# Performance work log

Hardware: AMD Instinct MI355X
Metric: run time of the kernel (lower is better)

Reference implementation:

```python
import jax, jax.numpy as jnp
import numpy as np


def setup_inputs() -> dict:
    key = jax.random.key(0)
    ks = jax.random.split(key, 7)
    T, B, I, H = 512, 64, 256, 512
    s_ih = 1.0 / np.sqrt(H)
    return {
        "x": jax.random.normal(ks[0], (T, B, I), dtype=jnp.float32),
        "h0": jax.random.normal(ks[1], (B, H), dtype=jnp.float32),
        "c0": jax.random.normal(ks[2], (B, H), dtype=jnp.float32),
        "w_ih": jax.random.normal(ks[3], (4 * H, I), dtype=jnp.float32) * s_ih,
        "w_hh": jax.random.normal(ks[4], (4 * H, H), dtype=jnp.float32) * s_ih,
        "b_ih": jax.random.normal(ks[5], (4 * H,), dtype=jnp.float32) * s_ih,
        "b_hh": jax.random.normal(ks[6], (4 * H,), dtype=jnp.float32) * s_ih,
    }


def reference(x, h0, c0, w_ih, w_hh, b_ih, b_hh):
    # Precompute the input projection for all timesteps in one big GEMM:
    # [T,B,I] @ [I,4H] -> [T,B,4H]
    xg = jnp.einsum("tbi,gi->tbg", x, w_ih) + b_ih + b_hh

    H = h0.shape[-1]

    def step(carry, xg_t):
        h, c = carry
        gates = xg_t + h @ w_hh.T  # [B, 4H]
        i_g, f_g, g_g, o_g = jnp.split(gates, 4, axis=-1)
        i_g = jax.nn.sigmoid(i_g)
        f_g = jax.nn.sigmoid(f_g)
        g_g = jnp.tanh(g_g)
        o_g = jax.nn.sigmoid(o_g)
        c_new = f_g * c + i_g * g_g
        h_new = o_g * jnp.tanh(c_new)
        return (h_new, c_new), h_new

    (h_f, c_f), outputs = jax.lax.scan(step, (h0, c0), xg)
    return outputs, h_f, c_f
```

## Files before the change

### kernel.cpp

```cpp
#include <hip/hip_runtime.h>
#include <hip/hip_bf16.h>

typedef __attribute__((ext_vector_type(8))) _Float16 half8;
typedef __attribute__((ext_vector_type(4))) float floatx4;
typedef __attribute__((ext_vector_type(4))) unsigned uintx4;

#define NTS 512
#define NB  64
#define NI  256
#define NH  512
#define NWG 128
#define NTHR 256

#define LOSCALE 4096.0f
#define LOINV   (1.0f / 4096.0f)

static __device__ __forceinline__ void split8s(const float* p, half8& hi, half8& lo) {
  float4 a = *(const float4*)p;
  float4 b = *(const float4*)(p + 4);
  float v[8] = {a.x, a.y, a.z, a.w, b.x, b.y, b.z, b.w};
#pragma unroll
  for (int i = 0; i < 8; ++i) {
    _Float16 h = (_Float16)v[i];
    hi[i] = h;
    lo[i] = (_Float16)((v[i] - (float)h) * LOSCALE);
  }
}

static __device__ __forceinline__ unsigned pack_cell_e(float v, unsigned ep) {
  _Float16 h = (_Float16)v;
  _Float16 l = (_Float16)((v - (float)h) * LOSCALE);
  union { _Float16 f; unsigned short s; } uh, ul;
  uh.f = h; ul.f = l;
  unsigned lo = ((unsigned)ul.s & 0xFFFCu) | (ep & 3u);
  return (lo << 16) | (unsigned)uh.s;
}

static __device__ __forceinline__ uintx4 load_cx4(const unsigned* p) {
  uintx4 r;
  asm volatile("global_load_dwordx4 %0, %1, off sc0 sc1"
               : "=v"(r)
               : "v"((unsigned long long)p)
               : "memory");
  return r;
}

__global__ void __launch_bounds__(NTHR, 1) lstm_persist_v10(
    const float* __restrict__ x,
    const float* __restrict__ h0,
    const float* __restrict__ c0,
    const float* __restrict__ w_ih,
    const float* __restrict__ w_hh,
    const float* __restrict__ b_ih,
    const float* __restrict__ b_hh,
    float* __restrict__ out,
    unsigned* __restrict__ hbuf)
{
  const int wg   = blockIdx.x;
  const int mh   = wg >> 5;
  const int ng   = wg & 31;
  const int b0   = mh * 16;
  const int j0   = ng * 16;
  const int tid  = threadIdx.x;
  const int wv   = tid >> 6;
  const int lane = tid & 63;
  const int ln   = lane & 15;
  const int lq   = lane >> 4;
  const int gL   = ln >> 2;
  const int cL   = ln & 3;

  __shared__ uintx4    wlo[4][24][64];
  __shared__ unsigned  hstage[16][516];

  int row_l[4];
  {
    half8 ones, rowv;
#pragma unroll
    for (int i = 0; i < 8; ++i) { ones[i] = (_Float16)1.0f; rowv[i] = (_Float16)(float)ln; }
    floatx4 z = {0.f, 0.f, 0.f, 0.f};
    floatx4 p1 = __builtin_amdgcn_mfma_f32_16x16x32_f16(rowv, ones, z, 0, 0, 0);
#pragma unroll
    for (int r = 0; r < 4; ++r)
      row_l[r] = (int)(p1[r] * (1.0f / 32.0f) + 0.5f);
  }

  const int jg   = j0 + wv * 4 + cL;
  const int grow = gL * NH + jg;
  half8 whh_hi[16], wih_hi[8];
  {
#pragma unroll
    for (int s = 0; s < 16; ++s) {
      half8 lo;
      split8s(w_hh + (size_t)grow * NH + 32 * s + 8 * lq, whh_hi[s], lo);
      union { half8 h; uintx4 u; } cv; cv.h = lo;
      wlo[wv][s][lane] = cv.u;
    }
#pragma unroll
    for (int s = 0; s < 8; ++s) {
      half8 lo;
      split8s(w_ih + (size_t)grow * NI + 32 * s + 8 * lq, wih_hi[s], lo);
      union { half8 h; uintx4 u; } cv; cv.h = lo;
      wlo[wv][16 + s][lane] = cv.u;
    }
  }

  const float bias_i = b_ih[jg]          + b_hh[jg];
  const float bias_f = b_ih[NH + jg]     + b_hh[NH + jg];
  const float bias_g = b_ih[2 * NH + jg] + b_hh[2 * NH + jg];
  const float bias_o = b_ih[3 * NH + jg] + b_hh[3 * NH + jg];

  int   bg_r[4];
  float c_s[4];
#pragma unroll
  for (int r = 0; r < 4; ++r) {
    bg_r[r] = b0 + row_l[r];
    c_s[r]  = c0[bg_r[r] * NH + jg];
  }

  const int PAR = NB * NH;

  if (gL == 0) {
#pragma unroll
    for (int r = 0; r < 4; ++r)
      __hip_atomic_store(&hbuf[bg_r[r] * NH + jg], pack_cell_e(h0[bg_r[r] * NH + jg], 0u),
                         __ATOMIC_RELAXED, __HIP_MEMORY_SCOPE_AGENT);
  }

  const int arow = b0 + ln;
  const int srow = tid & 15;
  const int scb  = (tid >> 4) * 32;

  for (int t = 0; t < NTS; ++t) {
    floatx4 acc_x   = {0.f, 0.f, 0.f, 0.f};
    floatx4 accl_x1 = {0.f, 0.f, 0.f, 0.f};
    floatx4 accl_x2 = {0.f, 0.f, 0.f, 0.f};
#pragma unroll
    for (int s = 0; s < 8; ++s) {
      half8 xh, xl;
      split8s(x + ((size_t)t * NB + arow) * NI + 32 * s + 8 * lq, xh, xl);
      union { uintx4 u; half8 h; } wl; wl.u = wlo[wv][16 + s][lane];
      acc_x   = __builtin_amdgcn_mfma_f32_16x16x32_f16(xh, wih_hi[s], acc_x,   0, 0, 0);
      accl_x1 = __builtin_amdgcn_mfma_f32_16x16x32_f16(xl, wih_hi[s], accl_x1, 0, 0, 0);
      accl_x2 = __builtin_amdgcn_mfma_f32_16x16x32_f16(xh, wl.h,      accl_x2, 0, 0, 0);
    }

    {
      const unsigned* hb = hbuf + (t & 1) * PAR + (b0 + srow) * NH + scb;
      const unsigned em = (unsigned)((t >> 1) & 3) << 16;
      uintx4 hv[8];
#pragma unroll
      for (int q = 0; q < 8; ++q) hv[q] = load_cx4(hb + 4 * q);

      __syncthreads();

      unsigned pend = 0xFFu;
      for (;;) {
        asm volatile("s_waitcnt vmcnt(0)" ::: "memory");
#pragma unroll
        for (int q = 0; q < 8; ++q) {
          if (pend & (1u << q)) {
            uintx4 v = hv[q];
            unsigned bad = ((v[0] ^ em) | (v[1] ^ em) | (v[2] ^ em) | (v[3] ^ em))
                           & 0x00030000u;
            if (!bad) {
              *(uintx4*)&hstage[srow][scb + 4 * q] = v;
              pend &= ~(1u << q);
            }
          }
        }
        if (__ballot(pend != 0u) == 0ull) break;
#pragma unroll
        for (int q = 0; q < 8; ++q)
          if (pend & (1u << q)) hv[q] = load_cx4(hb + 4 * q);
      }
    }
    __syncthreads();

    floatx4 acc_h  = {0.f, 0.f, 0.f, 0.f}, acc_h2  = {0.f, 0.f, 0.f, 0.f};
    floatx4 accl_a = {0.f, 0.f, 0.f, 0.f}, accl_a2 = {0.f, 0.f, 0.f, 0.f};
    floatx4 accl_b = {0.f, 0.f, 0.f, 0.f}, accl_b2 = {0.f, 0.f, 0.f, 0.f};
#pragma unroll
    for (int s = 0; s < 16; ++s) {
      const uintx4* hp = (const uintx4*)&hstage[ln][32 * s + 8 * lq];
      uintx4 hA = hp[0], hB = hp[1];
      union { unsigned u[4]; half8 h; } Ah, Al;
      Ah.u[0] = __builtin_amdgcn_perm(hA[1], hA[0], 0x05040100u);
      Al.u[0] = __builtin_amdgcn_perm(hA[1], hA[0], 0x07060302u);
      Ah.u[1] = __builtin_amdgcn_perm(hA[3], hA[2], 0x05040100u);
      Al.u[1] = __builtin_amdgcn_perm(hA[3], hA[2], 0x07060302u);
      Ah.u[2] = __builtin_amdgcn_perm(hB[1], hB[0], 0x05040100u);
      Al.u[2] = __builtin_amdgcn_perm(hB[1], hB[0], 0x07060302u);
      Ah.u[3] = __builtin_amdgcn_perm(hB[3], hB[2], 0x05040100u);
      Al.u[3] = __builtin_amdgcn_perm(hB[3], hB[2], 0x07060302u);
      union { uintx4 u; half8 h; } wl; wl.u = wlo[wv][s][lane];
      if (s < 8) {
        acc_h  = __builtin_amdgcn_mfma_f32_16x16x32_f16(Ah.h, whh_hi[s], acc_h,  0, 0, 0);
        accl_a = __builtin_amdgcn_mfma_f32_16x16x32_f16(Al.h, whh_hi[s], accl_a, 0, 0, 0);
        accl_b = __builtin_amdgcn_mfma_f32_16x16x32_f16(Ah.h, wl.h,      accl_b, 0, 0, 0);
      } else {
        acc_h2  = __builtin_amdgcn_mfma_f32_16x16x32_f16(Ah.h, whh_hi[s], acc_h2,  0, 0, 0);
        accl_a2 = __builtin_amdgcn_mfma_f32_16x16x32_f16(Al.h, whh_hi[s], accl_a2, 0, 0, 0);
        accl_b2 = __builtin_amdgcn_mfma_f32_16x16x32_f16(Ah.h, wl.h,      accl_b2, 0, 0, 0);
      }
    }

    const int par1 = ((t + 1) & 1) * PAR;
    const unsigned ep1 = (unsigned)(((t + 1) >> 1) & 3);
    float hn[4];
#pragma unroll
    for (int r = 0; r < 4; ++r) {
      float hi_s = acc_x[r] + acc_h[r] + acc_h2[r];
      float lo_s = accl_x1[r] + accl_x2[r] + accl_a[r] + accl_a2[r]
                 + accl_b[r] + accl_b2[r];
      float pre = hi_s + lo_s * LOINV;
      float pb = __shfl_xor(pre, 4);
      float pc = __shfl_xor(pre, 8);
      float pd = __shfl_xor(pb, 8);
      const bool g1 = (gL & 1), g2 = (gL & 2) != 0;
      float xi = g2 ? (g1 ? pd : pc) : (g1 ? pb : pre);
      float xf = g2 ? (g1 ? pc : pd) : (g1 ? pre : pb);
      float xg = g2 ? (g1 ? pb : pre) : (g1 ? pd : pc);
      float xo = g2 ? (g1 ? pre : pb) : (g1 ? pc : pd);
      xi += bias_i; xf += bias_f; xg += bias_g; xo += bias_o;
      float ig = 1.f / (1.f + __expf(-xi));
      float fg = 1.f / (1.f + __expf(-xf));
      float gg = 2.f / (1.f + __expf(-2.f * xg)) - 1.f;
      float og = 1.f / (1.f + __expf(-xo));
      c_s[r] = fg * c_s[r] + ig * gg;
      float tc = 2.f / (1.f + __expf(-2.f * c_s[r])) - 1.f;
      hn[r] = og * tc;
    }

    if (gL == 0) {
#pragma unroll
      for (int r = 0; r < 4; ++r)
        __hip_atomic_store(&hbuf[par1 + bg_r[r] * NH + jg], pack_cell_e(hn[r], ep1),
                           __ATOMIC_RELAXED, __HIP_MEMORY_SCOPE_AGENT);
    }

    if (gL == 0) {
      if (t < NTS - 1) {
#pragma unroll
        for (int r = 0; r < 4; ++r)
          out[((size_t)t * NB + bg_r[r]) * NH + jg] = hn[r];
      } else {
        const size_t hf_off = (size_t)NTS * NB * NH;
#pragma unroll
        for (int r = 0; r < 4; ++r) {
          out[((size_t)t * NB + bg_r[r]) * NH + jg] = hn[r];
          out[hf_off + bg_r[r] * NH + jg] = hn[r];
          out[hf_off + (size_t)NB * NH + bg_r[r] * NH + jg] = c_s[r];
        }
      }
    }
  }
}

extern "C" void kernel_launch(void* const* d_in, const int* in_sizes, int n_in,
                              void* d_out, int out_size, void* d_ws, size_t ws_size,
                              hipStream_t stream) {
  const float* x    = (const float*)d_in[0];
  const float* h0   = (const float*)d_in[1];
  const float* c0   = (const float*)d_in[2];
  const float* w_ih = (const float*)d_in[3];
  const float* w_hh = (const float*)d_in[4];
  const float* b_ih = (const float*)d_in[5];
  const float* b_hh = (const float*)d_in[6];
  float* out = (float*)d_out;
  unsigned* hbuf = (unsigned*)d_ws;

  hipLaunchKernelGGL(lstm_persist_v10, dim3(NWG), dim3(NTHR), 0, stream,
                     x, h0, c0, w_ih, w_hh, b_ih, b_hh, out, hbuf);
}
```

Baseline: 3.036 ms.

## Halve workgroup count with 8-wave blocks, swizzled h staging, vectorized h stores

Reorganizes the persistent LSTM from 128 workgroups of 4 waves to 64 workgroups of 8 waves, each covering 32 hidden units. This halves the number of blocks that must poll the shared h buffer each step. The W_ih low half now lives in registers instead of LDS, and the h-buffer loads are issued before the x-projection so they overlap it. The LDS h staging uses an XOR swizzle to avoid bank conflicts, and the new h values are transposed with lane shuffles so each thread writes a 16-byte packed store to both hbuf and the output. The cost is higher register pressure, heavier per-block work, and a new way of mapping lanes to stored rows.

```diff
diff --git a/kernel.cpp b/kernel.cpp
--- a/kernel.cpp
+++ b/kernel.cpp
@@ -9,8 +9,8 @@
 #define NB  64
 #define NI  256
 #define NH  512
-#define NWG 128
-#define NTHR 256
+#define NWG 64
+#define NTHR 512
 
 #define LOSCALE 4096.0f
 #define LOINV   (1.0f / 4096.0f)
@@ -44,8 +44,13 @@
                : "memory");
   return r;
 }
-
-__global__ void __launch_bounds__(NTHR, 1) lstm_persist_v10(
+static __device__ __forceinline__ void store_cx4(unsigned* p, uintx4 v) {
+  asm volatile("global_store_dwordx4 %0, %1, off sc0 sc1"
+               :: "v"((unsigned long long)p), "v"(v)
+               : "memory");
+}
+
+__global__ void __launch_bounds__(NTHR, 2) lstm_persist_v11(
     const float* __restrict__ x,
     const float* __restrict__ h0,
     const float* __restrict__ c0,
@@ -57,10 +62,10 @@
     unsigned* __restrict__ hbuf)
 {
   const int wg   = blockIdx.x;
-  const int mh   = wg >> 5;
-  const int ng   = wg & 31;
+  const int mh   = wg >> 4;
+  const int ng   = wg & 15;
   const int b0   = mh * 16;
-  const int j0   = ng * 16;
+  const int j0   = ng * 32;
   const int tid  = threadIdx.x;
   const int wv   = tid >> 6;
   const int lane = tid & 63;
@@ -69,8 +74,8 @@
   const int gL   = ln >> 2;
   const int cL   = ln & 3;
 
-  __shared__ uintx4    wlo[4][24][64];
-  __shared__ unsigned  hstage[16][516];
+  __shared__ uintx4    wlo[8][15][64];
+  __shared__ unsigned  hstage[16][512];
 
   int row_l[4];
   {
@@ -85,23 +90,24 @@
   }
 
   const int jg   = j0 + wv * 4 + cL;
+  const int jb   = j0 + wv * 4;
   const int grow = gL * NH + jg;
-  half8 whh_hi[16], wih_hi[8];
+  half8 whh_hi[16], wih_hi[8], wih_lo[8], whh_lo15;
   {
 #pragma unroll
     for (int s = 0; s < 16; ++s) {
       half8 lo;
       split8s(w_hh + (size_t)grow * NH + 32 * s + 8 * lq, whh_hi[s], lo);
-      union { half8 h; uintx4 u; } cv; cv.h = lo;
-      wlo[wv][s][lane] = cv.u;
-    }
-#pragma unroll
-    for (int s = 0; s < 8; ++s) {
-      half8 lo;
-      split8s(w_ih + (size_t)grow * NI + 32 * s + 8 * lq, wih_hi[s], lo);
-      union { half8 h; uintx4 u; } cv; cv.h = lo;
-      wlo[wv][16 + s][lane] = cv.u;
-    }
+      if (s < 15) {
+        union { half8 h; uintx4 u; } cv; cv.h = lo;
+        wlo[wv][s][lane] = cv.u;
+      } else {
+        whh_lo15 = lo;
+      }
+    }
+#pragma unroll
+    for (int s = 0; s < 8; ++s)
+      split8s(w_ih + (size_t)grow * NI + 32 * s + 8 * lq, wih_hi[s], wih_lo[s]);
   }
 
   const float bias_i = b_ih[jg]          + b_hh[jg];
@@ -116,6 +122,8 @@
     bg_r[r] = b0 + row_l[r];
     c_s[r]  = c0[bg_r[r] * NH + jg];
   }
+  const int brow_st = b0 + ((cL == 0) ? row_l[0] : (cL == 1) ? row_l[1]
+                           : (cL == 2) ? row_l[2] : row_l[3]);
 
   const int PAR = NB * NH;
 
@@ -126,11 +134,16 @@
                          __ATOMIC_RELAXED, __HIP_MEMORY_SCOPE_AGENT);
   }
 
-  const int arow = b0 + ln;
-  const int srow = tid & 15;
-  const int scb  = (tid >> 4) * 32;
+  const int arow  = b0 + ln;
+  const int srow  = tid & 15;
+  const int qbase = (tid >> 4) * 4;
 
   for (int t = 0; t < NTS; ++t) {
+    const unsigned* hb = hbuf + (t & 1) * PAR + (b0 + srow) * NH + qbase * 4;
+    uintx4 hv[4];
+#pragma unroll
+    for (int q = 0; q < 4; ++q) hv[q] = load_cx4(hb + 4 * q);
+
     floatx4 acc_x   = {0.f, 0.f, 0.f, 0.f};
     floatx4 accl_x1 = {0.f, 0.f, 0.f, 0.f};
     floatx4 accl_x2 = {0.f, 0.f, 0.f, 0.f};
@@ -138,39 +151,34 @@
     for (int s = 0; s < 8; ++s) {
       half8 xh, xl;
       split8s(x + ((size_t)t * NB + arow) * NI + 32 * s + 8 * lq, xh, xl);
-      union { uintx4 u; half8 h; } wl; wl.u = wlo[wv][16 + s][lane];
       acc_x   = __builtin_amdgcn_mfma_f32_16x16x32_f16(xh, wih_hi[s], acc_x,   0, 0, 0);
       accl_x1 = __builtin_amdgcn_mfma_f32_16x16x32_f16(xl, wih_hi[s], accl_x1, 0, 0, 0);
-      accl_x2 = __builtin_amdgcn_mfma_f32_16x16x32_f16(xh, wl.h,      accl_x2, 0, 0, 0);
-    }
+      accl_x2 = __builtin_amdgcn_mfma_f32_16x16x32_f16(xh, wih_lo[s], accl_x2, 0, 0, 0);
+    }
+
+    __syncthreads();
 
     {
-      const unsigned* hb = hbuf + (t & 1) * PAR + (b0 + srow) * NH + scb;
       const unsigned em = (unsigned)((t >> 1) & 3) << 16;
-      uintx4 hv[8];
-#pragma unroll
-      for (int q = 0; q < 8; ++q) hv[q] = load_cx4(hb + 4 * q);
-
-      __syncthreads();
-
-      unsigned pend = 0xFFu;
+      unsigned pend = 0xFu;
       for (;;) {
         asm volatile("s_waitcnt vmcnt(0)" ::: "memory");
 #pragma unroll
-        for (int q = 0; q < 8; ++q) {
+        for (int q = 0; q < 4; ++q) {
           if (pend & (1u << q)) {
             uintx4 v = hv[q];
             unsigned bad = ((v[0] ^ em) | (v[1] ^ em) | (v[2] ^ em) | (v[3] ^ em))
                            & 0x00030000u;
             if (!bad) {
-              *(uintx4*)&hstage[srow][scb + 4 * q] = v;
+              const int slot = (qbase + q) ^ (srow & 7);
+              *(uintx4*)&hstage[srow][slot << 2] = v;
               pend &= ~(1u << q);
             }
           }
         }
         if (__ballot(pend != 0u) == 0ull) break;
 #pragma unroll
-        for (int q = 0; q < 8; ++q)
+        for (int q = 0; q < 4; ++q)
           if (pend & (1u << q)) hv[q] = load_cx4(hb + 4 * q);
       }
     }
@@ -181,8 +189,9 @@
     floatx4 accl_b = {0.f, 0.f, 0.f, 0.f}, accl_b2 = {0.f, 0.f, 0.f, 0.f};
 #pragma unroll
     for (int s = 0; s < 16; ++s) {
-      const uintx4* hp = (const uintx4*)&hstage[ln][32 * s + 8 * lq];
-      uintx4 hA = hp[0], hB = hp[1];
+      const int q0 = 8 * s + 2 * lq;
+      uintx4 hA = *(const uintx4*)&hstage[ln][(q0 ^ (ln & 7)) << 2];
+      uintx4 hB = *(const uintx4*)&hstage[ln][((q0 + 1) ^ (ln & 7)) << 2];
       union { unsigned u[4]; half8 h; } Ah, Al;
       Ah.u[0] = __builtin_amdgcn_perm(hA[1], hA[0], 0x05040100u);
       Al.u[0] = __builtin_amdgcn_perm(hA[1], hA[0], 0x07060302u);
@@ -192,15 +201,21 @@
       Al.u[2] = __builtin_amdgcn_perm(hB[1], hB[0], 0x07060302u);
       Ah.u[3] = __builtin_amdgcn_perm(hB[3], hB[2], 0x05040100u);
       Al.u[3] = __builtin_amdgcn_perm(hB[3], hB[2], 0x07060302u);
-      union { uintx4 u; half8 h; } wl; wl.u = wlo[wv][s][lane];
+      half8 wlh;
+      if (s < 15) {
+        union { uintx4 u; half8 h; } wl; wl.u = wlo[wv][s][lane];
+        wlh = wl.h;
+      } else {
+        wlh = whh_lo15;
+      }
       if (s < 8) {
         acc_h  = __builtin_amdgcn_mfma_f32_16x16x32_f16(Ah.h, whh_hi[s], acc_h,  0, 0, 0);
         accl_a = __builtin_amdgcn_mfma_f32_16x16x32_f16(Al.h, whh_hi[s], accl_a, 0, 0, 0);
-        accl_b = __builtin_amdgcn_mfma_f32_16x16x32_f16(Ah.h, wl.h,      accl_b, 0, 0, 0);
+        accl_b = __builtin_amdgcn_mfma_f32_16x16x32_f16(Ah.h, wlh,       accl_b, 0, 0, 0);
       } else {
         acc_h2  = __builtin_amdgcn_mfma_f32_16x16x32_f16(Ah.h, whh_hi[s], acc_h2,  0, 0, 0);
         accl_a2 = __builtin_amdgcn_mfma_f32_16x16x32_f16(Al.h, whh_hi[s], accl_a2, 0, 0, 0);
-        accl_b2 = __builtin_amdgcn_mfma_f32_16x16x32_f16(Ah.h, wl.h,      accl_b2, 0, 0, 0);
+        accl_b2 = __builtin_amdgcn_mfma_f32_16x16x32_f16(Ah.h, wlh,       accl_b2, 0, 0, 0);
       }
     }
 
@@ -231,19 +246,29 @@
       hn[r] = og * tc;
     }
 
-    if (gL == 0) {
-#pragma unroll
-      for (int r = 0; r < 4; ++r)
-        __hip_atomic_store(&hbuf[par1 + bg_r[r] * NH + jg], pack_cell_e(hn[r], ep1),
-                           __ATOMIC_RELAXED, __HIP_MEMORY_SCOPE_AGENT);
-    }
-
-    if (gL == 0) {
-      if (t < NTS - 1) {
-#pragma unroll
-        for (int r = 0; r < 4; ++r)
-          out[((size_t)t * NB + bg_r[r]) * NH + jg] = hn[r];
-      } else {
+    if (t < NTS - 1) {
+      const bool c0b = (lane & 1), c1b = (lane & 2) != 0;
+      float a0 = __shfl_xor(hn[1], 1), a1 = __shfl_xor(hn[0], 1);
+      float a2 = __shfl_xor(hn[3], 1), a3 = __shfl_xor(hn[2], 1);
+      float v10 = c0b ? a0 : hn[0], v11 = c0b ? hn[1] : a1;
+      float v12 = c0b ? a2 : hn[2], v13 = c0b ? hn[3] : a3;
+      float b0v = __shfl_xor(v12, 2), b1v = __shfl_xor(v13, 2);
+      float b2v = __shfl_xor(v10, 2), b3v = __shfl_xor(v11, 2);
+      float T0 = c1b ? b0v : v10, T1 = c1b ? b1v : v11;
+      float T2 = c1b ? v12 : b2v, T3 = c1b ? v13 : b3v;
+
+      if (gL == 0) {
+        uintx4 pk;
+        pk[0] = pack_cell_e(T0, ep1);
+        pk[1] = pack_cell_e(T1, ep1);
+        pk[2] = pack_cell_e(T2, ep1);
+        pk[3] = pack_cell_e(T3, ep1);
+        store_cx4(&hbuf[par1 + brow_st * NH + jb], pk);
+        floatx4 ov = {T0, T1, T2, T3};
+        *(floatx4*)&out[((size_t)t * NB + brow_st) * NH + jb] = ov;
+      }
+    } else {
+      if (gL == 0) {
         const size_t hf_off = (size_t)NTS * NB * NH;
 #pragma unroll
         for (int r = 0; r < 4; ++r) {
@@ -269,6 +294,6 @@
   float* out = (float*)d_out;
   unsigned* hbuf = (unsigned*)d_ws;
 
-  hipLaunchKernelGGL(lstm_persist_v10, dim3(NWG), dim3(NTHR), 0, stream,
+  hipLaunchKernelGGL(lstm_persist_v11, dim3(NWG), dim3(NTHR), 0, stream,
                      x, h0, c0, w_ih, w_hh, b_ih, b_hh, out, hbuf);
 }
```

After: 6.326 ms. 108% more time.

## Prefetch h before x-projection, double-buffer spin polls, vectorize h stores via shuffles

Applied to the files above, without the earlier changes.

The first poll of the previous-step hidden state is now issued before the input-projection MFMAs, so its latency overlaps that compute. The spin-wait alternates two in-flight batches of loads using vmcnt(8) instead of draining everything on each retry. Per-lane scalar atomic stores of h and out are replaced by a lane-shuffle transpose and one 16-byte store per lane with sc0 sc1 cache bits. This cuts cross-workgroup handoff latency and store count, at the cost of more outstanding loads, extra shuffles, and reliance on the packed epoch tags staying consistent within a dwordx4 store.

```diff
diff --git a/kernel.cpp b/kernel.cpp
--- a/kernel.cpp
+++ b/kernel.cpp
@@ -44,8 +44,13 @@
                : "memory");
   return r;
 }
-
-__global__ void __launch_bounds__(NTHR, 1) lstm_persist_v10(
+static __device__ __forceinline__ void store_cx4(unsigned* p, uintx4 v) {
+  asm volatile("global_store_dwordx4 %0, %1, off sc0 sc1"
+               :: "v"((unsigned long long)p), "v"(v)
+               : "memory");
+}
+
+__global__ void __launch_bounds__(NTHR, 1) lstm_persist_v16(
     const float* __restrict__ x,
     const float* __restrict__ h0,
     const float* __restrict__ c0,
@@ -85,6 +90,7 @@
   }
 
   const int jg   = j0 + wv * 4 + cL;
+  const int jb   = j0 + wv * 4;
   const int grow = gL * NH + jg;
   half8 whh_hi[16], wih_hi[8];
   {
@@ -116,6 +122,8 @@
     bg_r[r] = b0 + row_l[r];
     c_s[r]  = c0[bg_r[r] * NH + jg];
   }
+  const int brow_st = b0 + ((cL == 0) ? row_l[0] : (cL == 1) ? row_l[1]
+                           : (cL == 2) ? row_l[2] : row_l[3]);
 
   const int PAR = NB * NH;
 
@@ -131,6 +139,11 @@
   const int scb  = (tid >> 4) * 32;
 
   for (int t = 0; t < NTS; ++t) {
+    const unsigned* hb = hbuf + (t & 1) * PAR + (b0 + srow) * NH + scb;
+    uintx4 hv[8];
+#pragma unroll
+    for (int q = 0; q < 8; ++q) hv[q] = load_cx4(hb + 4 * q);
+
     floatx4 acc_x   = {0.f, 0.f, 0.f, 0.f};
     floatx4 accl_x1 = {0.f, 0.f, 0.f, 0.f};
     floatx4 accl_x2 = {0.f, 0.f, 0.f, 0.f};
@@ -144,18 +157,17 @@
       accl_x2 = __builtin_amdgcn_mfma_f32_16x16x32_f16(xh, wl.h,      accl_x2, 0, 0, 0);
     }
 
+    __syncthreads();
+
     {
-      const unsigned* hb = hbuf + (t & 1) * PAR + (b0 + srow) * NH + scb;
       const unsigned em = (unsigned)((t >> 1) & 3) << 16;
-      uintx4 hv[8];
-#pragma unroll
-      for (int q = 0; q < 8; ++q) hv[q] = load_cx4(hb + 4 * q);
-
-      __syncthreads();
+      uintx4 hw[8];
+#pragma unroll
+      for (int q = 0; q < 8; ++q) hw[q] = load_cx4(hb + 4 * q);
 
       unsigned pend = 0xFFu;
       for (;;) {
-        asm volatile("s_waitcnt vmcnt(0)" ::: "memory");
+        asm volatile("s_waitcnt vmcnt(8)" ::: "memory");
 #pragma unroll
         for (int q = 0; q < 8; ++q) {
           if (pend & (1u << q)) {
@@ -170,9 +182,26 @@
         }
         if (__ballot(pend != 0u) == 0ull) break;
 #pragma unroll
-        for (int q = 0; q < 8; ++q)
-          if (pend & (1u << q)) hv[q] = load_cx4(hb + 4 * q);
+        for (int q = 0; q < 8; ++q) hv[q] = load_cx4(hb + 4 * q);
+
+        asm volatile("s_waitcnt vmcnt(8)" ::: "memory");
+#pragma unroll
+        for (int q = 0; q < 8; ++q) {
+          if (pend & (1u << q)) {
+            uintx4 v = hw[q];
+            unsigned bad = ((v[0] ^ em) | (v[1] ^ em) | (v[2] ^ em) | (v[3] ^ em))
+                           & 0x00030000u;
+            if (!bad) {
+              *(uintx4*)&hstage[srow][scb + 4 * q] = v;
+              pend &= ~(1u << q);
+            }
+          }
+        }
+        if (__ballot(pend != 0u) == 0ull) break;
+#pragma unroll
+        for (int q = 0; q < 8; ++q) hw[q] = load_cx4(hb + 4 * q);
       }
+      asm volatile("s_waitcnt vmcnt(0)" ::: "memory");
     }
     __syncthreads();
 
@@ -231,19 +260,29 @@
       hn[r] = og * tc;
     }
 
-    if (gL == 0) {
-#pragma unroll
-      for (int r = 0; r < 4; ++r)
-        __hip_atomic_store(&hbuf[par1 + bg_r[r] * NH + jg], pack_cell_e(hn[r], ep1),
-                           __ATOMIC_RELAXED, __HIP_MEMORY_SCOPE_AGENT);
-    }
-
-    if (gL == 0) {
-      if (t < NTS - 1) {
-#pragma unroll
-        for (int r = 0; r < 4; ++r)
-          out[((size_t)t * NB + bg_r[r]) * NH + jg] = hn[r];
-      } else {
+    if (t < NTS - 1) {
+      const bool c0b = (lane & 1), c1b = (lane & 2) != 0;
+      float a0 = __shfl_xor(hn[1], 1), a1 = __shfl_xor(hn[0], 1);
+      float a2 = __shfl_xor(hn[3], 1), a3 = __shfl_xor(hn[2], 1);
+      float v10 = c0b ? a0 : hn[0], v11 = c0b ? hn[1] : a1;
+      float v12 = c0b ? a2 : hn[2], v13 = c0b ? hn[3] : a3;
+      float b0v = __shfl_xor(v12, 2), b1v = __shfl_xor(v13, 2);
+      float b2v = __shfl_xor(v10, 2), b3v = __shfl_xor(v11, 2);
+      float T0 = c1b ? b0v : v10, T1 = c1b ? b1v : v11;
+      float T2 = c1b ? v12 : b2v, T3 = c1b ? v13 : b3v;
+
+      if (gL == 0) {
+        uintx4 pk;
+        pk[0] = pack_cell_e(T0, ep1);
+        pk[1] = pack_cell_e(T1, ep1);
+        pk[2] = pack_cell_e(T2, ep1);
+        pk[3] = pack_cell_e(T3, ep1);
+        store_cx4(&hbuf[par1 + brow_st * NH + jb], pk);
+        floatx4 ov = {T0, T1, T2, T3};
+        *(floatx4*)&out[((size_t)t * NB + brow_st) * NH + jb] = ov;
+      }
+    } else {
+      if (gL == 0) {
         const size_t hf_off = (size_t)NTS * NB * NH;
 #pragma unroll
         for (int r = 0; r < 4; ++r) {
@@ -269,6 +308,6 @@
   float* out = (float*)d_out;
   unsigned* hbuf = (unsigned*)d_ws;
 
-  hipLaunchKernelGGL(lstm_persist_v10, dim3(NWG), dim3(NTHR), 0, stream,
+  hipLaunchKernelGGL(lstm_persist_v16, dim3(NWG), dim3(NTHR), 0, stream,
                      x, h0, c0, w_ih, w_hh, b_ih, b_hh, out, hbuf);
 }
```

Result: slower. 4.910 ms (+61.7%).

## Halve workgroup count, give each wave two hidden-column tiles with vectorized h stores

Applied to the files above, without the earlier changes.

Cuts the persistent grid from 128 to 64 workgroups. Each wave now computes two 4-column hidden tiles, with the extra weight halves held in registers. The h-buffer loads for the next step are issued before the input-projection MFMAs so their latency overlaps that work. Per-lane results are transposed through lane shuffles so the recurrent state and outputs can be written as dwordx4 stores instead of scalar atomics. The aim is fewer participants in the per-step grid-wide handoff and more efficient stores, at the cost of doubling MFMA work and register pressure per workgroup on the serial critical path.

```diff
diff --git a/kernel.cpp b/kernel.cpp
--- a/kernel.cpp
+++ b/kernel.cpp
@@ -9,7 +9,7 @@
 #define NB  64
 #define NI  256
 #define NH  512
-#define NWG 128
+#define NWG 64
 #define NTHR 256
 
 #define LOSCALE 4096.0f
@@ -44,8 +44,13 @@
                : "memory");
   return r;
 }
-
-__global__ void __launch_bounds__(NTHR, 1) lstm_persist_v10(
+static __device__ __forceinline__ void store_cx4(unsigned* p, uintx4 v) {
+  asm volatile("global_store_dwordx4 %0, %1, off sc0 sc1"
+               :: "v"((unsigned long long)p), "v"(v)
+               : "memory");
+}
+
+__global__ void __launch_bounds__(NTHR, 1) lstm_persist_v17(
     const float* __restrict__ x,
     const float* __restrict__ h0,
     const float* __restrict__ c0,
@@ -57,10 +62,10 @@
     unsigned* __restrict__ hbuf)
 {
   const int wg   = blockIdx.x;
-  const int mh   = wg >> 5;
-  const int ng   = wg & 31;
+  const int mh   = wg >> 4;
+  const int ng   = wg & 15;
   const int b0   = mh * 16;
-  const int j0   = ng * 16;
+  const int j0   = ng * 32;
   const int tid  = threadIdx.x;
   const int wv   = tid >> 6;
   const int lane = tid & 63;
@@ -84,46 +89,62 @@
       row_l[r] = (int)(p1[r] * (1.0f / 32.0f) + 0.5f);
   }
 
-  const int jg   = j0 + wv * 4 + cL;
-  const int grow = gL * NH + jg;
-  half8 whh_hi[16], wih_hi[8];
+  const int jb    = j0 + wv * 8;
+  const int jga   = jb + cL;
+  const int jgb   = jb + 4 + cL;
+  const int growa = gL * NH + jga;
+  const int growb = gL * NH + jgb;
+  half8 whh_hi_a[16], whh_hi_b[16], whh_lo_a[16];
+  half8 wih_hi_a[8],  wih_hi_b[8],  wih_lo_a[8];
   {
 #pragma unroll
     for (int s = 0; s < 16; ++s) {
-      half8 lo;
-      split8s(w_hh + (size_t)grow * NH + 32 * s + 8 * lq, whh_hi[s], lo);
-      union { half8 h; uintx4 u; } cv; cv.h = lo;
+      split8s(w_hh + (size_t)growa * NH + 32 * s + 8 * lq, whh_hi_a[s], whh_lo_a[s]);
+      half8 lob;
+      split8s(w_hh + (size_t)growb * NH + 32 * s + 8 * lq, whh_hi_b[s], lob);
+      union { half8 h; uintx4 u; } cv; cv.h = lob;
       wlo[wv][s][lane] = cv.u;
     }
 #pragma unroll
     for (int s = 0; s < 8; ++s) {
-      half8 lo;
-      split8s(w_ih + (size_t)grow * NI + 32 * s + 8 * lq, wih_hi[s], lo);
-      union { half8 h; uintx4 u; } cv; cv.h = lo;
+      split8s(w_ih + (size_t)growa * NI + 32 * s + 8 * lq, wih_hi_a[s], wih_lo_a[s]);
+      half8 lob;
+      split8s(w_ih + (size_t)growb * NI + 32 * s + 8 * lq, wih_hi_b[s], lob);
+      union { half8 h; uintx4 u; } cv; cv.h = lob;
       wlo[wv][16 + s][lane] = cv.u;
     }
   }
 
-  const float bias_i = b_ih[jg]          + b_hh[jg];
-  const float bias_f = b_ih[NH + jg]     + b_hh[NH + jg];
-  const float bias_g = b_ih[2 * NH + jg] + b_hh[2 * NH + jg];
-  const float bias_o = b_ih[3 * NH + jg] + b_hh[3 * NH + jg];
+  const float bi_a = b_ih[jga]          + b_hh[jga];
+  const float bf_a = b_ih[NH + jga]     + b_hh[NH + jga];
+  const float bg_a = b_ih[2 * NH + jga] + b_hh[2 * NH + jga];
+  const float bo_a = b_ih[3 * NH + jga] + b_hh[3 * NH + jga];
+  const float bi_b = b_ih[jgb]          + b_hh[jgb];
+  const float bf_b = b_ih[NH + jgb]     + b_hh[NH + jgb];
+  const float bg_b = b_ih[2 * NH + jgb] + b_hh[2 * NH + jgb];
+  const float bo_b = b_ih[3 * NH + jgb] + b_hh[3 * NH + jgb];
 
   int   bg_r[4];
-  float c_s[4];
+  float cs_a[4], cs_b[4];
 #pragma unroll
   for (int r = 0; r < 4; ++r) {
     bg_r[r] = b0 + row_l[r];
-    c_s[r]  = c0[bg_r[r] * NH + jg];
-  }
+    cs_a[r] = c0[bg_r[r] * NH + jga];
+    cs_b[r] = c0[bg_r[r] * NH + jgb];
+  }
+  const int brow_st = b0 + ((cL == 0) ? row_l[0] : (cL == 1) ? row_l[1]
+                           : (cL == 2) ? row_l[2] : row_l[3]);
 
   const int PAR = NB * NH;
 
   if (gL == 0) {
 #pragma unroll
-    for (int r = 0; r < 4; ++r)
-      __hip_atomic_store(&hbuf[bg_r[r] * NH + jg], pack_cell_e(h0[bg_r[r] * NH + jg], 0u),
+    for (int r = 0; r < 4; ++r) {
+      __hip_atomic_store(&hbuf[bg_r[r] * NH + jga], pack_cell_e(h0[bg_r[r] * NH + jga], 0u),
                          __ATOMIC_RELAXED, __HIP_MEMORY_SCOPE_AGENT);
+      __hip_atomic_store(&hbuf[bg_r[r] * NH + jgb], pack_cell_e(h0[bg_r[r] * NH + jgb], 0u),
+                         __ATOMIC_RELAXED, __HIP_MEMORY_SCOPE_AGENT);
+    }
   }
 
   const int arow = b0 + ln;
@@ -131,28 +152,31 @@
   const int scb  = (tid >> 4) * 32;
 
   for (int t = 0; t < NTS; ++t) {
-    floatx4 acc_x   = {0.f, 0.f, 0.f, 0.f};
-    floatx4 accl_x1 = {0.f, 0.f, 0.f, 0.f};
-    floatx4 accl_x2 = {0.f, 0.f, 0.f, 0.f};
+    const unsigned* hb = hbuf + (t & 1) * PAR + (b0 + srow) * NH + scb;
+    uintx4 hv[8];
+#pragma unroll
+    for (int q = 0; q < 8; ++q) hv[q] = load_cx4(hb + 4 * q);
+
+    floatx4 acc_a  = {0.f, 0.f, 0.f, 0.f}, acc_b  = {0.f, 0.f, 0.f, 0.f};
+    floatx4 acl_a1 = {0.f, 0.f, 0.f, 0.f}, acl_b1 = {0.f, 0.f, 0.f, 0.f};
+    floatx4 acl_a2 = {0.f, 0.f, 0.f, 0.f}, acl_b2 = {0.f, 0.f, 0.f, 0.f};
 #pragma unroll
     for (int s = 0; s < 8; ++s) {
       half8 xh, xl;
       split8s(x + ((size_t)t * NB + arow) * NI + 32 * s + 8 * lq, xh, xl);
-      union { uintx4 u; half8 h; } wl; wl.u = wlo[wv][16 + s][lane];
-      acc_x   = __builtin_amdgcn_mfma_f32_16x16x32_f16(xh, wih_hi[s], acc_x,   0, 0, 0);
-      accl_x1 = __builtin_amdgcn_mfma_f32_16x16x32_f16(xl, wih_hi[s], accl_x1, 0, 0, 0);
-      accl_x2 = __builtin_amdgcn_mfma_f32_16x16x32_f16(xh, wl.h,      accl_x2, 0, 0, 0);
-    }
+      union { uintx4 u; half8 h; } wlb; wlb.u = wlo[wv][16 + s][lane];
+      acc_a  = __builtin_amdgcn_mfma_f32_16x16x32_f16(xh, wih_hi_a[s], acc_a,  0, 0, 0);
+      acl_a1 = __builtin_amdgcn_mfma_f32_16x16x32_f16(xl, wih_hi_a[s], acl_a1, 0, 0, 0);
+      acl_a2 = __builtin_amdgcn_mfma_f32_16x16x32_f16(xh, wih_lo_a[s], acl_a2, 0, 0, 0);
+      acc_b  = __builtin_amdgcn_mfma_f32_16x16x32_f16(xh, wih_hi_b[s], acc_b,  0, 0, 0);
+      acl_b1 = __builtin_amdgcn_mfma_f32_16x16x32_f16(xl, wih_hi_b[s], acl_b1, 0, 0, 0);
+      acl_b2 = __builtin_amdgcn_mfma_f32_16x16x32_f16(xh, wlb.h,       acl_b2, 0, 0, 0);
+    }
+
+    __syncthreads();
 
     {
-      const unsigned* hb = hbuf + (t & 1) * PAR + (b0 + srow) * NH + scb;
       const unsigned em = (unsigned)((t >> 1) & 3) << 16;
-      uintx4 hv[8];
-#pragma unroll
-      for (int q = 0; q < 8; ++q) hv[q] = load_cx4(hb + 4 * q);
-
-      __syncthreads();
-
       unsigned pend = 0xFFu;
       for (;;) {
         asm volatile("s_waitcnt vmcnt(0)" ::: "memory");
@@ -176,9 +200,6 @@
     }
     __syncthreads();
 
-    floatx4 acc_h  = {0.f, 0.f, 0.f, 0.f}, acc_h2  = {0.f, 0.f, 0.f, 0.f};
-    floatx4 accl_a = {0.f, 0.f, 0.f, 0.f}, accl_a2 = {0.f, 0.f, 0.f, 0.f};
-    floatx4 accl_b = {0.f, 0.f, 0.f, 0.f}, accl_b2 = {0.f, 0.f, 0.f, 0.f};
 #pragma unroll
     for (int s = 0; s < 16; ++s) {
       const uintx4* hp = (const uintx4*)&hstage[ln][32 * s + 8 * lq];
@@ -192,64 +213,102 @@
       Al.u[2] = __builtin_amdgcn_perm(hB[1], hB[0], 0x07060302u);
       Ah.u[3] = __builtin_amdgcn_perm(hB[3], hB[2], 0x05040100u);
       Al.u[3] = __builtin_amdgcn_perm(hB[3], hB[2], 0x07060302u);
-      union { uintx4 u; half8 h; } wl; wl.u = wlo[wv][s][lane];
-      if (s < 8) {
-        acc_h  = __builtin_amdgcn_mfma_f32_16x16x32_f16(Ah.h, whh_hi[s], acc_h,  0, 0, 0);
-        accl_a = __builtin_amdgcn_mfma_f32_16x16x32_f16(Al.h, whh_hi[s], accl_a, 0, 0, 0);
-        accl_b = __builtin_amdgcn_mfma_f32_16x16x32_f16(Ah.h, wl.h,      accl_b, 0, 0, 0);
-      } else {
-        acc_h2  = __builtin_amdgcn_mfma_f32_16x16x32_f16(Ah.h, whh_hi[s], acc_h2,  0, 0, 0);
-        accl_a2 = __builtin_amdgcn_mfma_f32_16x16x32_f16(Al.h, whh_hi[s], accl_a2, 0, 0, 0);
-        accl_b2 = __builtin_amdgcn_mfma_f32_16x16x32_f16(Ah.h, wl.h,      accl_b2, 0, 0, 0);
-      }
+      union { uintx4 u; half8 h; } wlb; wlb.u = wlo[wv][s][lane];
+      acc_a  = __builtin_amdgcn_mfma_f32_16x16x32_f16(Ah.h, whh_hi_a[s], acc_a,  0, 0, 0);
+      acl_a1 = __builtin_amdgcn_mfma_f32_16x16x32_f16(Al.h, whh_hi_a[s], acl_a1, 0, 0, 0);
+      acl_a2 = __builtin_amdgcn_mfma_f32_16x16x32_f16(Ah.h, whh_lo_a[s], acl_a2, 0, 0, 0);
+      acc_b  = __builtin_amdgcn_mfma_f32_16x16x32_f16(Ah.h, whh_hi_b[s], acc_b,  0, 0, 0);
+      acl_b1 = __builtin_amdgcn_mfma_f32_16x16x32_f16(Al.h, whh_hi_b[s], acl_b1, 0, 0, 0);
+      acl_b2 = __builtin_amdgcn_mfma_f32_16x16x32_f16(Ah.h, wlb.h,       acl_b2, 0, 0, 0);
     }
 
     const int par1 = ((t + 1) & 1) * PAR;
     const unsigned ep1 = (unsigned)(((t + 1) >> 1) & 3);
-    float hn[4];
+    const bool g1 = (gL & 1), g2 = (gL & 2) != 0;
+    float hn_a[4], hn_b[4];
 #pragma unroll
     for (int r = 0; r < 4; ++r) {
-      float hi_s = acc_x[r] + acc_h[r] + acc_h2[r];
-      float lo_s = accl_x1[r] + accl_x2[r] + accl_a[r] + accl_a2[r]
-                 + accl_b[r] + accl_b2[r];
-      float pre = hi_s + lo_s * LOINV;
-      float pb = __shfl_xor(pre, 4);
-      float pc = __shfl_xor(pre, 8);
-      float pd = __shfl_xor(pb, 8);
-      const bool g1 = (gL & 1), g2 = (gL & 2) != 0;
-      float xi = g2 ? (g1 ? pd : pc) : (g1 ? pb : pre);
-      float xf = g2 ? (g1 ? pc : pd) : (g1 ? pre : pb);
-      float xg = g2 ? (g1 ? pb : pre) : (g1 ? pd : pc);
-      float xo = g2 ? (g1 ? pre : pb) : (g1 ? pc : pd);
-      xi += bias_i; xf += bias_f; xg += bias_g; xo += bias_o;
-      float ig = 1.f / (1.f + __expf(-xi));
-      float fg = 1.f / (1.f + __expf(-xf));
-      float gg = 2.f / (1.f + __expf(-2.f * xg)) - 1.f;
-      float og = 1.f / (1.f + __expf(-xo));
-      c_s[r] = fg * c_s[r] + ig * gg;
-      float tc = 2.f / (1.f + __expf(-2.f * c_s[r])) - 1.f;
-      hn[r] = og * tc;
-    }
-
-    if (gL == 0) {
-#pragma unroll
-      for (int r = 0; r < 4; ++r)
-        __hip_atomic_store(&hbuf[par1 + bg_r[r] * NH + jg], pack_cell_e(hn[r], ep1),
-                           __ATOMIC_RELAXED, __HIP_MEMORY_SCOPE_AGENT);
-    }
-
-    if (gL == 0) {
-      if (t < NTS - 1) {
-#pragma unroll
-        for (int r = 0; r < 4; ++r)
-          out[((size_t)t * NB + bg_r[r]) * NH + jg] = hn[r];
-      } else {
+      {
+        float pre = (acc_a[r]) + (acl_a1[r] + acl_a2[r]) * LOINV;
+        float pb = __shfl_xor(pre, 4);
+        float pc = __shfl_xor(pre, 8);
+        float pd = __shfl_xor(pb, 8);
+        float xi = g2 ? (g1 ? pd : pc) : (g1 ? pb : pre);
+        float xf = g2 ? (g1 ? pc : pd) : (g1 ? pre : pb);
+        float xg = g2 ? (g1 ? pb : pre) : (g1 ? pd : pc);
+        float xo = g2 ? (g1 ? pre : pb) : (g1 ? pc : pd);
+        xi += bi_a; xf += bf_a; xg += bg_a; xo += bo_a;
+        float ig = 1.f / (1.f + __expf(-xi));
+        float fg = 1.f / (1.f + __expf(-xf));
+        float gg = 2.f / (1.f + __expf(-2.f * xg)) - 1.f;
+        float og = 1.f / (1.f + __expf(-xo));
+        cs_a[r] = fg * cs_a[r] + ig * gg;
+        float tc = 2.f / (1.f + __expf(-2.f * cs_a[r])) - 1.f;
+        hn_a[r] = og * tc;
+      }
+      {
+        float pre = (acc_b[r]) + (acl_b1[r] + acl_b2[r]) * LOINV;
+        float pb = __shfl_xor(pre, 4);
+        float pc = __shfl_xor(pre, 8);
+        float pd = __shfl_xor(pb, 8);
+        float xi = g2 ? (g1 ? pd : pc) : (g1 ? pb : pre);
+        float xf = g2 ? (g1 ? pc : pd) : (g1 ? pre : pb);
+        float xg = g2 ? (g1 ? pb : pre) : (g1 ? pd : pc);
+        float xo = g2 ? (g1 ? pre : pb) : (g1 ? pc : pd);
+        xi += bi_b; xf += bf_b; xg += bg_b; xo += bo_b;
+        float ig = 1.f / (1.f + __expf(-xi));
+        float fg = 1.f / (1.f + __expf(-xf));
+        float gg = 2.f / (1.f + __expf(-2.f * xg)) - 1.f;
+        float og = 1.f / (1.f + __expf(-xo));
+        cs_b[r] = fg * cs_b[r] + ig * gg;
+        float tc = 2.f / (1.f + __expf(-2.f * cs_b[r])) - 1.f;
+        hn_b[r] = og * tc;
+      }
+    }
+
+    if (t < NTS - 1) {
+      const bool c0b = (lane & 1), c1b = (lane & 2) != 0;
+      float a0 = __shfl_xor(hn_a[1], 1), a1 = __shfl_xor(hn_a[0], 1);
+      float a2 = __shfl_xor(hn_a[3], 1), a3 = __shfl_xor(hn_a[2], 1);
+      float v10 = c0b ? a0 : hn_a[0], v11 = c0b ? hn_a[1] : a1;
+      float v12 = c0b ? a2 : hn_a[2], v13 = c0b ? hn_a[3] : a3;
+      float b0v = __shfl_xor(v12, 2), b1v = __shfl_xor(v13, 2);
+      float b2v = __shfl_xor(v10, 2), b3v = __shfl_xor(v11, 2);
+      float TA0 = c1b ? b0v : v10, TA1 = c1b ? b1v : v11;
+      float TA2 = c1b ? v12 : b2v, TA3 = c1b ? v13 : b3v;
+      float d0 = __shfl_xor(hn_b[1], 1), d1 = __shfl_xor(hn_b[0], 1);
+      float d2 = __shfl_xor(hn_b[3], 1), d3 = __shfl_xor(hn_b[2], 1);
+      float w10 = c0b ? d0 : hn_b[0], w11 = c0b ? hn_b[1] : d1;
+      float w12 = c0b ? d2 : hn_b[2], w13 = c0b ? hn_b[3] : d3;
+      float e0v = __shfl_xor(w12, 2), e1v = __shfl_xor(w13, 2);
+      float e2v = __shfl_xor(w10, 2), e3v = __shfl_xor(w11, 2);
+      float TB0 = c1b ? e0v : w10, TB1 = c1b ? e1v : w11;
+      float TB2 = c1b ? w12 : e2v, TB3 = c1b ? w13 : e3v;
+
+      if (gL == 0) {
+        uintx4 pa, pbq;
+        pa[0] = pack_cell_e(TA0, ep1); pa[1] = pack_cell_e(TA1, ep1);
+        pa[2] = pack_cell_e(TA2, ep1); pa[3] = pack_cell_e(TA3, ep1);
+        pbq[0] = pack_cell_e(TB0, ep1); pbq[1] = pack_cell_e(TB1, ep1);
+        pbq[2] = pack_cell_e(TB2, ep1); pbq[3] = pack_cell_e(TB3, ep1);
+        store_cx4(&hbuf[par1 + brow_st * NH + jb],     pa);
+        store_cx4(&hbuf[par1 + brow_st * NH + jb + 4], pbq);
+        floatx4 oa = {TA0, TA1, TA2, TA3};
+        floatx4 ob = {TB0, TB1, TB2, TB3};
+        *(floatx4*)&out[((size_t)t * NB + brow_st) * NH + jb]     = oa;
+        *(floatx4*)&out[((size_t)t * NB + brow_st) * NH + jb + 4] = ob;
+      }
+    } else {
+      if (gL == 0) {
         const size_t hf_off = (size_t)NTS * NB * NH;
 #pragma unroll
         for (int r = 0; r < 4; ++r) {
-          out[((size_t)t * NB + bg_r[r]) * NH + jg] = hn[r];
-          out[hf_off + bg_r[r] * NH + jg] = hn[r];
-          out[hf_off + (size_t)NB * NH + bg_r[r] * NH + jg] = c_s[r];
+          out[((size_t)t * NB + bg_r[r]) * NH + jga] = hn_a[r];
+          out[((size_t)t * NB + bg_r[r]) * NH + jgb] = hn_b[r];
+          out[hf_off + bg_r[r] * NH + jga] = hn_a[r];
+          out[hf_off + bg_r[r] * NH + jgb] = hn_b[r];
+          out[hf_off + (size_t)NB * NH + bg_r[r] * NH + jga] = cs_a[r];
+          out[hf_off + (size_t)NB * NH + bg_r[r] * NH + jgb] = cs_b[r];
         }
       }
     }
@@ -269,6 +328,6 @@
   float* out = (float*)d_out;
   unsigned* hbuf = (unsigned*)d_ws;
 
-  hipLaunchKernelGGL(lstm_persist_v10, dim3(NWG), dim3(NTHR), 0, stream,
+  hipLaunchKernelGGL(lstm_persist_v17, dim3(NWG), dim3(NTHR), 0, stream,
                      x, h0, c0, w_ih, w_hh, b_ih, b_hh, out, hbuf);
 }
```

New measurement: 4.864 ms. 1.6x slower.
